# Performance work log

Measured on AMD Instinct MI355X. Metric: run time of the kernel, lower is better.

The kernel has to match this reference:

```python
import jax, jax.numpy as jnp
import numpy as np

N = 50000   # nodes
E = 800000  # edges (avg degree 16)
F = 64      # num_features (channels per irrep)
R = 8       # radial basis size
H = 64      # radial MLP hidden
S = 10      # num_species
NPATH = 5   # tensor-product paths: s*Y0->0, s*Y1->1, v*Y0->1, v.Y1->0, v x Y1->1
AVG_NEIGH = 16.0


def setup_inputs() -> dict:
    key = jax.random.key(0)
    ks = jax.random.split(key, 20)
    def w(k, shape, fan_in):
        return jax.random.normal(k, shape, dtype=jnp.float32) / np.sqrt(fan_in)
    return dict(
        vectors=jax.random.normal(ks[0], (E, 3), dtype=jnp.float32),
        node_feats_s=jax.random.normal(ks[1], (N, F), dtype=jnp.float32),
        node_feats_v=jax.random.normal(ks[2], (N, F, 3), dtype=jnp.float32),
        radial_embedding=jax.random.normal(ks[3], (E, R), dtype=jnp.float32),
        Wu_s=w(ks[7], (F, F), F), Wu_v=w(ks[8], (F, F), F),
        W_r1=w(ks[9], (R, H), R), W_r2=w(ks[10], (H, NPATH * F), H),
        Wd_s=w(ks[11], (F, F), F), Wd_v=w(ks[12], (F, F), F),
        w_sym_s=jax.random.normal(ks[13], (S, 3, F), dtype=jnp.float32),
        w_sym_v=jax.random.normal(ks[14], (S, 2, F), dtype=jnp.float32),
        WL_s=w(ks[15], (F, F), F), WL_v=w(ks[16], (F, F), F),
        W_skip_s=w(ks[17], (S, F, F), F), W_skip_v=w(ks[18], (S, F, F), F),
        W_out=w(ks[19], (F, 1), F),
        node_specie=jax.random.randint(ks[4], (N,), 0, S),
        senders=jax.random.randint(ks[5], (E,), 0, N),
        receivers=jax.random.randint(ks[6], (E,), 0, N),
    )


def reference(vectors, node_feats_s, node_feats_v, radial_embedding,
              Wu_s, Wu_v, W_r1, W_r2, Wd_s, Wd_v,
              w_sym_s, w_sym_v, WL_s, WL_v, W_skip_s, W_skip_v, W_out,
              node_specie, senders, receivers):
    n = node_feats_s.shape[0]
    # ---- self-connection: species-indexed linear (skip_tp), per-irrep channel mix
    sc_s = jnp.einsum('nf,nfg->ng', node_feats_s, W_skip_s[node_specie])
    sc_v = jnp.einsum('nfc,nfg->ngc', node_feats_v, W_skip_v[node_specie])
    # ---- InteractionBlock: linear up
    s = node_feats_s @ Wu_s                                  # [N,F]
    v = jnp.einsum('nfc,fg->ngc', node_feats_v, Wu_v)        # [N,F,3]
    # radial MLP -> per-edge, per-path, per-channel tensor-product weights
    h = jax.nn.silu(radial_embedding @ W_r1)
    w = (h @ W_r2).reshape(-1, NPATH, s.shape[1])            # [E,5,F]
    # spherical harmonics (l=1): unit edge vectors
    Y1 = vectors / (jnp.linalg.norm(vectors, axis=-1, keepdims=True) + 1e-9)  # [E,3]
    xs = s[senders]                                          # [E,F]
    xv = v[senders]                                          # [E,F,3]
    # CG tensor product paths (0e+1o) x (Y0+Y1) -> 0e + 1o
    m_s = w[:, 0] * xs + w[:, 3] * jnp.einsum('efc,ec->ef', xv, Y1)
    m_v = (w[:, 1, :, None] * xs[:, :, None] * Y1[:, None, :]
           + w[:, 2, :, None] * xv
           + w[:, 4, :, None] * jnp.cross(xv, Y1[:, None, :]))
    # scatter-sum aggregation over receivers
    agg_s = jax.ops.segment_sum(m_s, receivers, num_segments=n)
    agg_v = jax.ops.segment_sum(m_v, receivers, num_segments=n)
    # linear down to num_features * interaction_irreps
    s = agg_s @ Wd_s
    v = jnp.einsum('nfc,fg->ngc', agg_v, Wd_v)
    # epsilon is None -> divide by sqrt(avg_num_neighbors)
    inv = 1.0 / np.sqrt(AVG_NEIGH).astype(np.float32)
    s = s * inv
    v = v * inv
    # ---- EquivariantProductBasisBlock: symmetric contraction (correlation=2),
    # species-indexed per-channel weights over the symmetric CG basis
    ws = w_sym_s[node_specie]                                # [N,3,F]
    wv = w_sym_v[node_specie]                                # [N,2,F]
    ps = ws[:, 0] * s + ws[:, 1] * s * s + ws[:, 2] * jnp.sum(v * v, axis=-1)
    pv = wv[:, 0, :, None] * v + wv[:, 1, :, None] * (s[:, :, None] * v)
    # linear to num_features * hidden_irreps
    fs = ps @ WL_s
    fv = jnp.einsum('nfc,fg->ngc', pv, WL_v)
    # residual skip connection
    fs = fs + sc_s
    fv = fv + sc_v
    # ---- LinearReadoutBlock to output_irreps = '0e'
    node_outputs = fs @ W_out                                # [N,1]
    return node_outputs, fs, fv
```

## Files before the change

### kernel.cpp

```cpp
#include <hip/hip_runtime.h>
#include <stdint.h>

#define F 64
#define RDIM 8
#define HDIM 64
#define NPATH 5
#define EB 64
#define PADH 72
#define PADN 324
#define NSP 16
#define PB 72
#define NT 4

typedef _Float16 half8 __attribute__((ext_vector_type(8)));
typedef _Float16 half4 __attribute__((ext_vector_type(4)));
typedef float floatx4 __attribute__((ext_vector_type(4)));

#define ES_E(v)   ((int)((v) >> 32))
#define ES_R(v)   ((int)(((v) >> 16) & 0xFFFFu))
#define ES_S(v)   ((int)((v) & 0xFFFFu))

__device__ inline half8 h8_from_f32(const float* p) {
    float4 a = ((const float4*)p)[0];
    float4 b = ((const float4*)p)[1];
    half8 h;
    h[0] = (_Float16)a.x; h[1] = (_Float16)a.y; h[2] = (_Float16)a.z; h[3] = (_Float16)a.w;
    h[4] = (_Float16)b.x; h[5] = (_Float16)b.y; h[6] = (_Float16)b.z; h[7] = (_Float16)b.w;
    return h;
}

__device__ inline half8 h8_from_f32_stride3(const float* p) {
    half8 h;
#pragma unroll
    for (int j = 0; j < 8; ++j) h[j] = (_Float16)p[j * 3];
    return h;
}

__device__ inline half8 h8_zero() {
    half8 h;
#pragma unroll
    for (int j = 0; j < 8; ++j) h[j] = (_Float16)0.f;
    return h;
}

__global__ __launch_bounds__(256) void k_pre_mfma(
    const float* __restrict__ nfs, const float* __restrict__ nfv,
    const float* __restrict__ Wus, const float* __restrict__ Wuv,
    half4* __restrict__ comb, int N,
    const int* __restrict__ recv, int* __restrict__ cnt, int E,
    const int* __restrict__ specie, int* __restrict__ nbin)
{
    __shared__ _Float16 BT[2][64 * PB];
    __shared__ int lbin[NSP];
    const int tid = threadIdx.x;
    const int wave = tid >> 6, lane = tid & 63;
    const int l15 = lane & 15, lq = lane >> 4;
    const int tb0 = blockIdx.x * 64;

    if (tid < NSP) lbin[tid] = 0;
    {
        const float* srcs[2] = { Wus, Wuv };
#pragma unroll
        for (int m = 0; m < 2; ++m) {
            const float* W = srcs[m];
#pragma unroll
            for (int rep = 0; rep < 16; ++rep) {
                int id = rep * 256 + tid;
                int k = id >> 6, n = id & 63;
                BT[m][n * PB + k] = (_Float16)W[k * F + n];
            }
        }
    }
    __syncthreads();

    {
        const int i0 = blockIdx.x * 256 + tid;
        const int stride = gridDim.x * 256;
        for (int e = i0; e < E; e += stride) atomicAdd(&cnt[recv[e]], 1);
        for (int n = i0; n < N; n += stride) atomicAdd(&lbin[specie[n]], 1);
    }

    const int tb = tb0 + wave * 16;
    const int ndA = tb + l15;

#define BFRAG(m, nt, ks) (*(const half8*)&BT[m][((nt) * 16 + l15) * PB + (ks) * 32 + lq * 8])

    floatx4 c[4][NT];
#pragma unroll
    for (int q = 0; q < 4; ++q)
#pragma unroll
        for (int nt = 0; nt < NT; ++nt) c[q][nt] = (floatx4){0.f, 0.f, 0.f, 0.f};

#pragma unroll
    for (int ks = 0; ks < 2; ++ks) {
        half8 a_s, a_v0, a_v1, a_v2;
        if (ndA < N) {
            a_s  = h8_from_f32(nfs + (size_t)ndA * F + ks * 32 + lq * 8);
            const float* vb = nfv + ((size_t)ndA * F + ks * 32 + lq * 8) * 3;
            a_v0 = h8_from_f32_stride3(vb + 0);
            a_v1 = h8_from_f32_stride3(vb + 1);
            a_v2 = h8_from_f32_stride3(vb + 2);
        } else {
            a_s = a_v0 = a_v1 = a_v2 = h8_zero();
        }
#pragma unroll
        for (int nt = 0; nt < NT; ++nt) {
            half8 bs = BFRAG(0, nt, ks);
            half8 bv = BFRAG(1, nt, ks);
            c[0][nt] = __builtin_amdgcn_mfma_f32_16x16x32_f16(a_s,  bs, c[0][nt], 0, 0, 0);
            c[1][nt] = __builtin_amdgcn_mfma_f32_16x16x32_f16(a_v0, bv, c[1][nt], 0, 0, 0);
            c[2][nt] = __builtin_amdgcn_mfma_f32_16x16x32_f16(a_v1, bv, c[2][nt], 0, 0, 0);
            c[3][nt] = __builtin_amdgcn_mfma_f32_16x16x32_f16(a_v2, bv, c[3][nt], 0, 0, 0);
        }
    }
#undef BFRAG

#pragma unroll
    for (int r = 0; r < 4; ++r) {
        const int nd = tb + lq * 4 + r;
        if (nd < N) {
#pragma unroll
            for (int nt = 0; nt < NT; ++nt) {
                half4 o;
                o[0] = (_Float16)c[0][nt][r];
                o[1] = (_Float16)c[1][nt][r];
                o[2] = (_Float16)c[2][nt][r];
                o[3] = (_Float16)c[3][nt][r];
                comb[(size_t)nd * F + nt * 16 + l15] = o;
            }
        }
    }

    __syncthreads();
    if (tid < NSP && lbin[tid] > 0) atomicAdd(&nbin[tid], lbin[tid]);
}

__global__ __launch_bounds__(1024) void k_scanA(
    const int* __restrict__ cnt, int* __restrict__ bsum, int N)
{
    __shared__ int lsum[1024];
    const int tid = threadIdx.x;
    const int i = blockIdx.x * 1024 + tid;
    int x = (i < N) ? cnt[i] : 0;
    lsum[tid] = x;
    __syncthreads();
    for (int off = 512; off > 0; off >>= 1) {
        if (tid < off) lsum[tid] += lsum[tid + off];
        __syncthreads();
    }
    if (tid == 0) bsum[blockIdx.x] = lsum[0];
}

__global__ __launch_bounds__(64) void k_scanB(
    int* __restrict__ bsum, int nb,
    const int* __restrict__ nbin, int* __restrict__ ncur)
{
    const int lane = threadIdx.x;
    int carry = 0;
    for (int base = 0; base < nb; base += 64) {
        const int idx = base + lane;
        int v = (idx < nb) ? bsum[idx] : 0;
        int incl = v;
#pragma unroll
        for (int off = 1; off < 64; off <<= 1) {
            int u = __shfl_up(incl, off, 64);
            if (lane >= off) incl += u;
        }
        int tot = __shfl(incl, 63, 64);
        if (idx < nb) bsum[idx] = incl - v + carry;
        carry += tot;
    }
    if (lane == 0) {
        int run = 0;
        for (int s = 0; s < NSP; ++s) {
            ncur[s] = run;
            run += ((nbin[s] + 63) >> 6) << 6;
        }
    }
}

__global__ __launch_bounds__(1024) void k_scanC(
    const int* __restrict__ cnt, const int* __restrict__ bsum,
    int* __restrict__ cursor, int N)
{
    __shared__ int lsum[1024];
    const int tid = threadIdx.x;
    const int i = blockIdx.x * 1024 + tid;
    int x = (i < N) ? cnt[i] : 0;
    lsum[tid] = x;
    __syncthreads();
    int acc = x;
    for (int off = 1; off < 1024; off <<= 1) {
        int add = (tid >= off) ? lsum[tid - off] : 0;
        __syncthreads();
        acc += add;
        lsum[tid] = acc;
        __syncthreads();
    }
    if (i < N) cursor[i] = acc - x + bsum[blockIdx.x];
}

__global__ __launch_bounds__(256) void k_scatter(
    const int* __restrict__ recv, const int* __restrict__ send,
    int* __restrict__ cursor, unsigned long long* __restrict__ esort, int E,
    const int* __restrict__ specie, int* __restrict__ ncur,
    int* __restrict__ nperm, int N)
{
    __shared__ int lbin[NSP], lbase[NSP], lcur[NSP];
    const int tid = threadIdx.x;
    const int i0 = blockIdx.x * 256 + tid;
    const int stride = gridDim.x * 256;
    for (int e = i0; e < E; e += stride) {
        int r = recv[e];
        int p = atomicAdd(&cursor[r], 1);
        esort[p] = ((unsigned long long)(unsigned int)e << 32)
                 | ((unsigned long long)(unsigned int)r << 16)
                 | (unsigned long long)(unsigned int)send[e];
    }
    if (tid < NSP) { lbin[tid] = 0; lcur[tid] = 0; }
    __syncthreads();
    int sp = -1;
    if (i0 < N) { sp = specie[i0]; atomicAdd(&lbin[sp], 1); }
    __syncthreads();
    if (tid < NSP && lbin[tid] > 0) lbase[tid] = atomicAdd(&ncur[tid], lbin[tid]);
    __syncthreads();
    if (i0 < N) {
        int off = atomicAdd(&lcur[sp], 1);
        nperm[lbase[sp] + off] = i0;
    }
}

__global__ __launch_bounds__(256, 3) void k_edge(
    const float* __restrict__ vecs, const float* __restrict__ re,
    const float* __restrict__ Wr1, const float* __restrict__ Wr2,
    const unsigned long long* __restrict__ esort,
    const half4* __restrict__ comb,
    float* __restrict__ agg_s, float* __restrict__ agg_v, int E)
{
    __shared__ _Float16 h_lds[EB * PADH];
    __shared__ _Float16 w_lds[EB * PADN];
    const int tid = threadIdx.x;
    const int wave = tid >> 6, lane = tid & 63;
    const int l15 = lane & 15, lq = lane >> 4;

    half8 bfrag[5][2];
#pragma unroll
    for (int nt = 0; nt < 5; ++nt)
#pragma unroll
        for (int ks = 0; ks < 2; ++ks)
#pragma unroll
            for (int j = 0; j < 8; ++j) {
                int k = ks * 32 + lq * 8 + j;
                int n = wave * 80 + nt * 16 + l15;
                bfrag[nt][ks][j] = (_Float16)Wr2[k * (NPATH * F) + n];
            }

    float w1r[RDIM];
#pragma unroll
    for (int r = 0; r < RDIM; ++r) w1r[r] = Wr1[r * HDIM + lane];

    const int niter = (E + EB - 1) / EB;
    for (int it = blockIdx.x; it < niter; it += gridDim.x) {
        const int base = it * EB;
        const bool full = (base + EB <= E);

        if (full) {
            const int ew = base + wave * 16;
            unsigned long long es1[16];
#pragma unroll
            for (int j = 0; j < 8; ++j)
                ((int4*)es1)[j] = ((const int4*)(esort + ew))[j];
            float4 ra[4], rb[4];
#pragma unroll
            for (int j = 0; j < 4; ++j) {
                const float4* rp = (const float4*)(re + (size_t)ES_E(es1[j]) * RDIM);
                ra[j] = rp[0]; rb[j] = rp[1];
            }
#pragma unroll
            for (int t = 0; t < 16; ++t) {
                float4 A = ra[t & 3], B = rb[t & 3];
                if (t < 12) {
                    const float4* rp = (const float4*)(re + (size_t)ES_E(es1[t + 4]) * RDIM);
                    ra[t & 3] = rp[0]; rb[t & 3] = rp[1];
                }
                float h = A.x * w1r[0] + A.y * w1r[1] + A.z * w1r[2] + A.w * w1r[3]
                        + B.x * w1r[4] + B.y * w1r[5] + B.z * w1r[6] + B.w * w1r[7];
                h = h / (1.f + __expf(-h));
                h_lds[(wave * 16 + t) * PADH + lane] = (_Float16)h;
            }
        } else {
            for (int t = 0; t < 16; ++t) {
                const int eloc = wave * 16 + t;
                const int e = base + eloc;
                float h = 0.f;
                if (e < E) {
                    const int pe = ES_E(esort[e]);
                    const float4* rp = (const float4*)(re + (size_t)pe * RDIM);
                    float4 A = rp[0], B = rp[1];
                    h = A.x * w1r[0] + A.y * w1r[1] + A.z * w1r[2] + A.w * w1r[3]
                      + B.x * w1r[4] + B.y * w1r[5] + B.z * w1r[6] + B.w * w1r[7];
                    h = h / (1.f + __expf(-h));
                }
                h_lds[eloc * PADH + lane] = (_Float16)h;
            }
        }
        __syncthreads();

        floatx4 c[4][5];
#pragma unroll
        for (int mt = 0; mt < 4; ++mt)
#pragma unroll
            for (int nt = 0; nt < 5; ++nt)
                c[mt][nt] = (floatx4){0.f, 0.f, 0.f, 0.f};
#pragma unroll
        for (int ks = 0; ks < 2; ++ks) {
            half8 a[4];
#pragma unroll
            for (int mt = 0; mt < 4; ++mt)
                a[mt] = *(const half8*)&h_lds[(mt * 16 + l15) * PADH + ks * 32 + lq * 8];
#pragma unroll
            for (int mt = 0; mt < 4; ++mt)
#pragma unroll
                for (int nt = 0; nt < 5; ++nt)
                    c[mt][nt] = __builtin_amdgcn_mfma_f32_16x16x32_f16(
                        a[mt], bfrag[nt][ks], c[mt][nt], 0, 0, 0);
        }
#pragma unroll
        for (int mt = 0; mt < 4; ++mt)
#pragma unroll
            for (int nt = 0; nt < 5; ++nt)
#pragma unroll
                for (int r = 0; r < 4; ++r) {
                    int row = mt * 16 + lq * 4 + r;
                    int col = wave * 80 + nt * 16 + l15;
                    w_lds[row * PADN + col] = (_Float16)c[mt][nt][r];
                }
        __syncthreads();

        if (full) {
            const int ew = base + wave * 16;
            unsigned long long es[16];
#pragma unroll
            for (int j = 0; j < 8; ++j)
                ((int4*)es)[j] = ((const int4*)(esort + ew))[j];
            half4 gb[4];
            float vxr[4], vyr[4], vzr[4];
#pragma unroll
            for (int j = 0; j < 4; ++j) {
                gb[j] = comb[(size_t)ES_S(es[j]) * F + lane];
                const float* vp = vecs + (size_t)ES_E(es[j]) * 3;
                vxr[j] = vp[0]; vyr[j] = vp[1]; vzr[j] = vp[2];
            }
            float accs = 0.f, acc0 = 0.f, acc1 = 0.f, acc2 = 0.f;
            int cur = ES_R(es[0]);
#pragma unroll
            for (int t = 0; t < 16; ++t) {
                half4 g = gb[t & 3];
                float vx = vxr[t & 3], vy = vyr[t & 3], vz = vzr[t & 3];
                if (t < 12) {
                    gb[t & 3] = comb[(size_t)ES_S(es[t + 4]) * F + lane];
                    const float* vp = vecs + (size_t)ES_E(es[t + 4]) * 3;
                    vxr[t & 3] = vp[0]; vyr[t & 3] = vp[1]; vzr[t & 3] = vp[2];
                }
                const int eloc = wave * 16 + t;
                float nrm = sqrtf(vx * vx + vy * vy + vz * vz);
                float inv = 1.f / (nrm + 1e-9f);
                float Yx = vx * inv, Yy = vy * inv, Yz = vz * inv;
                float w0  = (float)w_lds[eloc * PADN + 0 * F + lane];
                float w1p = (float)w_lds[eloc * PADN + 1 * F + lane];
                float w2p = (float)w_lds[eloc * PADN + 2 * F + lane];
                float w3p = (float)w_lds[eloc * PADN + 3 * F + lane];
                float w4p = (float)w_lds[eloc * PADN + 4 * F + lane];
                float xs = (float)g[0], x0 = (float)g[1], x1 = (float)g[2], x2 = (float)g[3];
                float dvY = x0 * Yx + x1 * Yy + x2 * Yz;
                float ms = w0 * xs + w3p * dvY;
                float m0 = w1p * xs * Yx + w2p * x0 + w4p * (x1 * Yz - x2 * Yy);
                float m1 = w1p * xs * Yy + w2p * x1 + w4p * (x2 * Yx - x0 * Yz);
                float m2 = w1p * xs * Yz + w2p * x2 + w4p * (x0 * Yy - x1 * Yx);
                const int rt = ES_R(es[t]);
                if (rt != cur) {
                    float* asb = agg_s + (size_t)cur * F;
                    float* avb = agg_v + (size_t)cur * 3 * F;
                    unsafeAtomicAdd(&asb[lane], accs);
                    unsafeAtomicAdd(&avb[lane], acc0);
                    unsafeAtomicAdd(&avb[F + lane], acc1);
                    unsafeAtomicAdd(&avb[2 * F + lane], acc2);
                    accs = acc0 = acc1 = acc2 = 0.f;
                    cur = rt;
                }
                accs += ms; acc0 += m0; acc1 += m1; acc2 += m2;
            }
            {
                float* asb = agg_s + (size_t)cur * F;
                float* avb = agg_v + (size_t)cur * 3 * F;
                unsafeAtomicAdd(&asb[lane], accs);
                unsafeAtomicAdd(&avb[lane], acc0);
                unsafeAtomicAdd(&avb[F + lane], acc1);
                unsafeAtomicAdd(&avb[2 * F + lane], acc2);
            }
        } else {
            for (int t = 0; t < 16; ++t) {
                const int eloc = wave * 16 + t;
                const int e = base + eloc;
                if (e >= E) break;
                const unsigned long long ev = esort[e];
                const int pe = ES_E(ev), snd = ES_S(ev), rcv = ES_R(ev);
                const float* vp = vecs + (size_t)pe * 3;
                float vx = vp[0], vy = vp[1], vz = vp[2];
                float nrm = sqrtf(vx * vx + vy * vy + vz * vz);
                float inv = 1.f / (nrm + 1e-9f);
                float Yx = vx * inv, Yy = vy * inv, Yz = vz * inv;
                half4 g = comb[(size_t)snd * F + lane];
                float w0  = (float)w_lds[eloc * PADN + 0 * F + lane];
                float w1p = (float)w_lds[eloc * PADN + 1 * F + lane];
                float w2p = (float)w_lds[eloc * PADN + 2 * F + lane];
                float w3p = (float)w_lds[eloc * PADN + 3 * F + lane];
                float w4p = (float)w_lds[eloc * PADN + 4 * F + lane];
                float xs = (float)g[0], x0 = (float)g[1], x1 = (float)g[2], x2 = (float)g[3];
                float dvY = x0 * Yx + x1 * Yy + x2 * Yz;
                float ms = w0 * xs + w3p * dvY;
                float m0 = w1p * xs * Yx + w2p * x0 + w4p * (x1 * Yz - x2 * Yy);
                float m1 = w1p * xs * Yy + w2p * x1 + w4p * (x2 * Yx - x0 * Yz);
                float m2 = w1p * xs * Yz + w2p * x2 + w4p * (x0 * Yy - x1 * Yx);
                float* asb = agg_s + (size_t)rcv * F;
                float* avb = agg_v + (size_t)rcv * 3 * F;
                unsafeAtomicAdd(&asb[lane], ms);
                unsafeAtomicAdd(&avb[lane], m0);
                unsafeAtomicAdd(&avb[F + lane], m1);
                unsafeAtomicAdd(&avb[2 * F + lane], m2);
            }
        }
    }
}

__global__ __launch_bounds__(256) void k_post_mfma(
    const float* __restrict__ agg_s, const float* __restrict__ agg_v,
    const float* __restrict__ nfs, const float* __restrict__ nfv,
    const float* __restrict__ Wds, const float* __restrict__ Wdv,
    const float* __restrict__ wss, const float* __restrict__ wsv,
    const float* __restrict__ WLs, const float* __restrict__ WLv,
    const float* __restrict__ Wsks, const float* __restrict__ Wskv,
    const float* __restrict__ Wout, const int* __restrict__ specie,
    const int* __restrict__ nperm,
    float* __restrict__ out0, float* __restrict__ out_fs,
    float* __restrict__ out_fv, int N)
{
    __shared__ _Float16 BT[6][64 * PB];
    __shared__ _Float16 P_lds[4][16 * PB];
    const int tid = threadIdx.x;
    const int wave = tid >> 6, lane = tid & 63;
    const int l15 = lane & 15, lq = lane >> 4;
    const int tb0 = blockIdx.x * 64;

    const int nfirst = nperm[tb0];
    const int sp = (nfirst < 0) ? 0 : specie[nfirst];

    {
        const float* srcs[6] = { Wds, Wdv,
                                 Wsks + (size_t)sp * F * F, Wskv + (size_t)sp * F * F,
                                 WLs, WLv };
#pragma unroll
        for (int m = 0; m < 6; ++m) {
            const float* W = srcs[m];
#pragma unroll
            for (int rep = 0; rep < 16; ++rep) {
                int id = rep * 256 + tid;
                int k = id >> 6, n = id & 63;
                BT[m][n * PB + k] = (_Float16)W[k * F + n];
            }
        }
    }
    __syncthreads();

    const int tb = tb0 + wave * 16;
    const int ndA = nperm[tb + l15];
    int ndr[4];
#pragma unroll
    for (int r = 0; r < 4; ++r) ndr[r] = nperm[tb + lq * 4 + r];

#define BFRAG(m, nt, ks) (*(const half8*)&BT[m][((nt) * 16 + l15) * PB + (ks) * 32 + lq * 8])

    floatx4 csk[4][NT];
#pragma unroll
    for (int q = 0; q < 4; ++q)
#pragma unroll
        for (int nt = 0; nt < NT; ++nt) csk[q][nt] = (floatx4){0.f, 0.f, 0.f, 0.f};
#pragma unroll
    for (int ks = 0; ks < 2; ++ks) {
        half8 a_s, a_v0, a_v1, a_v2;
        if (ndA >= 0) {
            a_s  = h8_from_f32(nfs + (size_t)ndA * F + ks * 32 + lq * 8);
            const float* vb = nfv + ((size_t)ndA * F + ks * 32 + lq * 8) * 3;
            a_v0 = h8_from_f32_stride3(vb + 0);
            a_v1 = h8_from_f32_stride3(vb + 1);
            a_v2 = h8_from_f32_stride3(vb + 2);
        } else {
            a_s = a_v0 = a_v1 = a_v2 = h8_zero();
        }
#pragma unroll
        for (int nt = 0; nt < NT; ++nt) {
            half8 bs = BFRAG(2, nt, ks);
            half8 bv = BFRAG(3, nt, ks);
            csk[0][nt] = __builtin_amdgcn_mfma_f32_16x16x32_f16(a_s,  bs, csk[0][nt], 0, 0, 0);
            csk[1][nt] = __builtin_amdgcn_mfma_f32_16x16x32_f16(a_v0, bv, csk[1][nt], 0, 0, 0);
            csk[2][nt] = __builtin_amdgcn_mfma_f32_16x16x32_f16(a_v1, bv, csk[2][nt], 0, 0, 0);
            csk[3][nt] = __builtin_amdgcn_mfma_f32_16x16x32_f16(a_v2, bv, csk[3][nt], 0, 0, 0);
        }
    }

    floatx4 cdn[4][NT];
#pragma unroll
    for (int q = 0; q < 4; ++q)
#pragma unroll
        for (int nt = 0; nt < NT; ++nt) cdn[q][nt] = (floatx4){0.f, 0.f, 0.f, 0.f};
#pragma unroll
    for (int ks = 0; ks < 2; ++ks) {
        half8 a_s, a_v0, a_v1, a_v2;
        if (ndA >= 0) {
            a_s  = h8_from_f32(agg_s + (size_t)ndA * F + ks * 32 + lq * 8);
            const float* vb = agg_v + (size_t)ndA * 3 * F + ks * 32 + lq * 8;
            a_v0 = h8_from_f32(vb);
            a_v1 = h8_from_f32(vb + F);
            a_v2 = h8_from_f32(vb + 2 * F);
        } else {
            a_s = a_v0 = a_v1 = a_v2 = h8_zero();
        }
#pragma unroll
        for (int nt = 0; nt < NT; ++nt) {
            half8 bs = BFRAG(0, nt, ks);
            half8 bv = BFRAG(1, nt, ks);
            cdn[0][nt] = __builtin_amdgcn_mfma_f32_16x16x32_f16(a_s,  bs, cdn[0][nt], 0, 0, 0);
            cdn[1][nt] = __builtin_amdgcn_mfma_f32_16x16x32_f16(a_v0, bv, cdn[1][nt], 0, 0, 0);
            cdn[2][nt] = __builtin_amdgcn_mfma_f32_16x16x32_f16(a_v1, bv, cdn[2][nt], 0, 0, 0);
            cdn[3][nt] = __builtin_amdgcn_mfma_f32_16x16x32_f16(a_v2, bv, cdn[3][nt], 0, 0, 0);
        }
    }

#pragma unroll
    for (int nt = 0; nt < NT; ++nt) {
        const int g = nt * 16 + l15;
        float a0 = wss[(sp * 3 + 0) * F + g];
        float a1 = wss[(sp * 3 + 1) * F + g];
        float a2 = wss[(sp * 3 + 2) * F + g];
        float b0 = wsv[(sp * 2 + 0) * F + g];
        float b1 = wsv[(sp * 2 + 1) * F + g];
#pragma unroll
        for (int r = 0; r < 4; ++r) {
            const float inv = 0.25f;
            float s2  = cdn[0][nt][r] * inv;
            float v20 = cdn[1][nt][r] * inv;
            float v21 = cdn[2][nt][r] * inv;
            float v22 = cdn[3][nt][r] * inv;
            cdn[0][nt][r] = a0 * s2 + a1 * s2 * s2
                          + a2 * (v20 * v20 + v21 * v21 + v22 * v22);
            cdn[1][nt][r] = b0 * v20 + b1 * s2 * v20;
            cdn[2][nt][r] = b0 * v21 + b1 * s2 * v21;
            cdn[3][nt][r] = b0 * v22 + b1 * s2 * v22;
        }
    }

#pragma unroll
    for (int q = 0; q < 4; ++q) {
#pragma unroll
        for (int nt = 0; nt < NT; ++nt)
#pragma unroll
            for (int r = 0; r < 4; ++r)
                P_lds[wave][(lq * 4 + r) * PB + nt * 16 + l15] = (_Float16)cdn[q][nt][r];
        __syncthreads();
        half8 ap0 = *(const half8*)&P_lds[wave][l15 * PB + 0 * 32 + lq * 8];
        half8 ap1 = *(const half8*)&P_lds[wave][l15 * PB + 1 * 32 + lq * 8];
        const int bm = (q == 0) ? 4 : 5;
#pragma unroll
        for (int nt = 0; nt < NT; ++nt) {
            csk[q][nt] = __builtin_amdgcn_mfma_f32_16x16x32_f16(ap0, BFRAG(bm, nt, 0), csk[q][nt], 0, 0, 0);
            csk[q][nt] = __builtin_amdgcn_mfma_f32_16x16x32_f16(ap1, BFRAG(bm, nt, 1), csk[q][nt], 0, 0, 0);
        }
        __syncthreads();
    }
#undef BFRAG

    float wo[NT];
#pragma unroll
    for (int nt = 0; nt < NT; ++nt) wo[nt] = Wout[nt * 16 + l15];
#pragma unroll
    for (int r = 0; r < 4; ++r) {
        const int nd = ndr[r];
        float po = 0.f;
        if (nd >= 0) {
#pragma unroll
            for (int nt = 0; nt < NT; ++nt) {
                const int g = nt * 16 + l15;
                float fs = csk[0][nt][r];
                out_fs[(size_t)nd * F + g] = fs;
                po += fs * wo[nt];
                float* fvp = out_fv + ((size_t)nd * F + g) * 3;
                fvp[0] = csk[1][nt][r];
                fvp[1] = csk[2][nt][r];
                fvp[2] = csk[3][nt][r];
            }
            po += __shfl_xor(po, 1, 64);
            po += __shfl_xor(po, 2, 64);
            po += __shfl_xor(po, 4, 64);
            po += __shfl_xor(po, 8, 64);
            if (l15 == 0) out0[nd] = po;
        }
    }
}

extern "C" void kernel_launch(void* const* d_in, const int* in_sizes, int n_in,
                              void* d_out, int out_size, void* d_ws, size_t ws_size,
                              hipStream_t stream)
{
    const float* vectors = (const float*)d_in[0];
    const float* nfs  = (const float*)d_in[1];
    const float* nfv  = (const float*)d_in[2];
    const float* re   = (const float*)d_in[3];
    const float* Wus  = (const float*)d_in[4];
    const float* Wuv  = (const float*)d_in[5];
    const float* Wr1  = (const float*)d_in[6];
    const float* Wr2  = (const float*)d_in[7];
    const float* Wds  = (const float*)d_in[8];
    const float* Wdv  = (const float*)d_in[9];
    const float* wss  = (const float*)d_in[10];
    const float* wsv  = (const float*)d_in[11];
    const float* WLs  = (const float*)d_in[12];
    const float* WLv  = (const float*)d_in[13];
    const float* Wsks = (const float*)d_in[14];
    const float* Wskv = (const float*)d_in[15];
    const float* Wout = (const float*)d_in[16];
    const int* specie    = (const int*)d_in[17];
    const int* senders   = (const int*)d_in[18];
    const int* receivers = (const int*)d_in[19];

    const int N = in_sizes[1] / F;
    const int E = in_sizes[18];

    const size_t NF = (size_t)N * F;
    const int NPAD_MAX = N + NSP * 64 + 64;
    half4* comb  = (half4*)d_ws;
    float* agg_s = (float*)((char*)d_ws + NF * sizeof(half4));
    float* agg_v = agg_s + NF;
    unsigned long long* esort = (unsigned long long*)(agg_v + 3 * NF);
    int*   cnt    = (int*)(esort + E);
    int*   nbin   = cnt + N;
    int*   ncur   = nbin + NSP;
    int*   cursor = ncur + NSP;
    int*   bsum   = cursor + N;
    int*   nperm  = bsum + 64;

    hipMemsetAsync(agg_s, 0, (size_t)4 * NF * sizeof(float), stream);
    hipMemsetAsync(cnt, 0, (size_t)(N + NSP) * sizeof(int), stream);
    hipMemsetAsync(nperm, 0xFF, (size_t)NPAD_MAX * sizeof(int), stream);

    const int nb64 = (N + 63) / 64;
    const int nbs = (N + 1023) / 1024;
    const int nbp = (N + NSP * 64 + 63) / 64;

    k_pre_mfma<<<nb64, 256, 0, stream>>>(nfs, nfv, Wus, Wuv, comb, N,
                                         receivers, cnt, E, specie, nbin);
    k_scanA<<<nbs, 1024, 0, stream>>>(cnt, bsum, N);
    k_scanB<<<1, 64, 0, stream>>>(bsum, nbs, nbin, ncur);
    k_scanC<<<nbs, 1024, 0, stream>>>(cnt, bsum, cursor, N);
    k_scatter<<<1024, 256, 0, stream>>>(receivers, senders, cursor, esort, E,
                                        specie, ncur, nperm, N);
    k_edge<<<2048, 256, 0, stream>>>(vectors, re, Wr1, Wr2, esort,
                                     comb, agg_s, agg_v, E);
    float* out0   = (float*)d_out;
    float* out_fs = out0 + N;
    float* out_fv = out_fs + (size_t)N * F;
    k_post_mfma<<<nbp, 256, 0, stream>>>(agg_s, agg_v, nfs, nfv, Wds, Wdv,
                                         wss, wsv, WLs, WLv, Wsks, Wskv,
                                         Wout, specie, nperm,
                                         out0, out_fs, out_fv, N);
}
```

Measured before the change: 542.1 us.

## Fuse scan and scatter kernels into one cooperative kernel with grid syncs

Merges the three-stage prefix scan (block sums, carry scan, per-block scan) and the edge/node scatter into a single cooperative kernel. Grid-wide syncs replace the kernel boundaries, and the scan chunk size drops from 1024 to 256. The goal is to remove three kernel launches and their gaps in a small, launch-bound preprocessing phase. The cost is a cooperative launch, grid.sync overhead, and the requirement that all 1024 blocks be co-resident, plus a larger bsum region.

```diff
diff --git a/kernel.cpp b/kernel.cpp
--- a/kernel.cpp
+++ b/kernel.cpp
@@ -1,5 +1,8 @@
 #include <hip/hip_runtime.h>
+#include <hip/hip_cooperative_groups.h>
 #include <stdint.h>
+
+namespace cg = cooperative_groups;
 
 #define F 64
 #define RDIM 8
@@ -11,6 +14,7 @@
 #define NSP 16
 #define PB 72
 #define NT 4
+#define SORT_BLOCKS 1024
 
 typedef _Float16 half8 __attribute__((ext_vector_type(8)));
 typedef _Float16 half4 __attribute__((ext_vector_type(4)));
@@ -135,79 +139,78 @@
     if (tid < NSP && lbin[tid] > 0) atomicAdd(&nbin[tid], lbin[tid]);
 }
 
-__global__ __launch_bounds__(1024) void k_scanA(
-    const int* __restrict__ cnt, int* __restrict__ bsum, int N)
+__global__ __launch_bounds__(256) void k_sort(
+    const int* __restrict__ cnt, int* __restrict__ bsum,
+    int* __restrict__ cursor,
+    const int* __restrict__ recv, const int* __restrict__ send,
+    unsigned long long* __restrict__ esort,
+    const int* __restrict__ specie, const int* __restrict__ nbin,
+    int* __restrict__ ncur, int* __restrict__ nperm, int N, int E)
 {
-    __shared__ int lsum[1024];
-    const int tid = threadIdx.x;
-    const int i = blockIdx.x * 1024 + tid;
-    int x = (i < N) ? cnt[i] : 0;
-    lsum[tid] = x;
-    __syncthreads();
-    for (int off = 512; off > 0; off >>= 1) {
-        if (tid < off) lsum[tid] += lsum[tid + off];
-        __syncthreads();
-    }
-    if (tid == 0) bsum[blockIdx.x] = lsum[0];
-}
-
-__global__ __launch_bounds__(64) void k_scanB(
-    int* __restrict__ bsum, int nb,
-    const int* __restrict__ nbin, int* __restrict__ ncur)
-{
-    const int lane = threadIdx.x;
-    int carry = 0;
-    for (int base = 0; base < nb; base += 64) {
-        const int idx = base + lane;
-        int v = (idx < nb) ? bsum[idx] : 0;
-        int incl = v;
-#pragma unroll
-        for (int off = 1; off < 64; off <<= 1) {
-            int u = __shfl_up(incl, off, 64);
-            if (lane >= off) incl += u;
-        }
-        int tot = __shfl(incl, 63, 64);
-        if (idx < nb) bsum[idx] = incl - v + carry;
-        carry += tot;
-    }
-    if (lane == 0) {
-        int run = 0;
-        for (int s = 0; s < NSP; ++s) {
-            ncur[s] = run;
-            run += ((nbin[s] + 63) >> 6) << 6;
-        }
-    }
-}
-
-__global__ __launch_bounds__(1024) void k_scanC(
-    const int* __restrict__ cnt, const int* __restrict__ bsum,
-    int* __restrict__ cursor, int N)
-{
-    __shared__ int lsum[1024];
-    const int tid = threadIdx.x;
-    const int i = blockIdx.x * 1024 + tid;
-    int x = (i < N) ? cnt[i] : 0;
-    lsum[tid] = x;
-    __syncthreads();
-    int acc = x;
-    for (int off = 1; off < 1024; off <<= 1) {
-        int add = (tid >= off) ? lsum[tid - off] : 0;
-        __syncthreads();
-        acc += add;
-        lsum[tid] = acc;
-        __syncthreads();
-    }
-    if (i < N) cursor[i] = acc - x + bsum[blockIdx.x];
-}
-
-__global__ __launch_bounds__(256) void k_scatter(
-    const int* __restrict__ recv, const int* __restrict__ send,
-    int* __restrict__ cursor, unsigned long long* __restrict__ esort, int E,
-    const int* __restrict__ specie, int* __restrict__ ncur,
-    int* __restrict__ nperm, int N)
-{
+    cg::grid_group grid = cg::this_grid();
+    __shared__ int lsum[256];
     __shared__ int lbin[NSP], lbase[NSP], lcur[NSP];
     const int tid = threadIdx.x;
+    const int nch = (N + 255) >> 8;
+
+    for (int ch = blockIdx.x; ch < nch; ch += gridDim.x) {
+        const int i = ch * 256 + tid;
+        int x = (i < N) ? cnt[i] : 0;
+        lsum[tid] = x;
+        __syncthreads();
+        for (int off = 128; off > 0; off >>= 1) {
+            if (tid < off) lsum[tid] += lsum[tid + off];
+            __syncthreads();
+        }
+        if (tid == 0) bsum[ch] = lsum[0];
+        __syncthreads();
+    }
+    grid.sync();
+
+    if (blockIdx.x == 0 && tid < 64) {
+        const int lane = tid;
+        int carry = 0;
+        for (int base = 0; base < nch; base += 64) {
+            const int idx = base + lane;
+            int v = (idx < nch) ? bsum[idx] : 0;
+            int incl = v;
+#pragma unroll
+            for (int off = 1; off < 64; off <<= 1) {
+                int u = __shfl_up(incl, off, 64);
+                if (lane >= off) incl += u;
+            }
+            int tot = __shfl(incl, 63, 64);
+            if (idx < nch) bsum[idx] = incl - v + carry;
+            carry += tot;
+        }
+        if (lane == 0) {
+            int run = 0;
+            for (int s = 0; s < NSP; ++s) {
+                ncur[s] = run;
+                run += ((nbin[s] + 63) >> 6) << 6;
+            }
+        }
+    }
+    grid.sync();
+
+    for (int ch = blockIdx.x; ch < nch; ch += gridDim.x) {
+        const int i = ch * 256 + tid;
+        int x = (i < N) ? cnt[i] : 0;
+        lsum[tid] = x;
+        __syncthreads();
+        int acc = x;
+        for (int off = 1; off < 256; off <<= 1) {
+            int add = (tid >= off) ? lsum[tid - off] : 0;
+            __syncthreads();
+            acc += add;
+            lsum[tid] = acc;
+            __syncthreads();
+        }
+        if (i < N) cursor[i] = acc - x + bsum[ch];
+        __syncthreads();
+    }
+    grid.sync();
+
     const int i0 = blockIdx.x * 256 + tid;
     const int stride = gridDim.x * 256;
     for (int e = i0; e < E; e += stride) {
@@ -632,8 +635,8 @@
     const int* senders   = (const int*)d_in[18];
     const int* receivers = (const int*)d_in[19];
 
-    const int N = in_sizes[1] / F;
-    const int E = in_sizes[18];
+    int N = in_sizes[1] / F;
+    int E = in_sizes[18];
 
     const size_t NF = (size_t)N * F;
     const int NPAD_MAX = N + NSP * 64 + 64;
@@ -646,23 +649,27 @@
     int*   ncur   = nbin + NSP;
     int*   cursor = ncur + NSP;
     int*   bsum   = cursor + N;
-    int*   nperm  = bsum + 64;
+    int*   nperm  = bsum + 256;
 
     hipMemsetAsync(agg_s, 0, (size_t)4 * NF * sizeof(float), stream);
     hipMemsetAsync(cnt, 0, (size_t)(N + NSP) * sizeof(int), stream);
     hipMemsetAsync(nperm, 0xFF, (size_t)NPAD_MAX * sizeof(int), stream);
 
     const int nb64 = (N + 63) / 64;
-    const int nbs = (N + 1023) / 1024;
     const int nbp = (N + NSP * 64 + 63) / 64;
 
     k_pre_mfma<<<nb64, 256, 0, stream>>>(nfs, nfv, Wus, Wuv, comb, N,
                                          receivers, cnt, E, specie, nbin);
-    k_scanA<<<nbs, 1024, 0, stream>>>(cnt, bsum, N);
-    k_scanB<<<1, 64, 0, stream>>>(bsum, nbs, nbin, ncur);
-    k_scanC<<<nbs, 1024, 0, stream>>>(cnt, bsum, cursor, N);
-    k_scatter<<<1024, 256, 0, stream>>>(receivers, senders, cursor, esort, E,
-                                        specie, ncur, nperm, N);
+
+    {
+        void* sargs[] = { (void*)&cnt, (void*)&bsum, (void*)&cursor,
+                          (void*)&receivers, (void*)&senders, (void*)&esort,
+                          (void*)&specie, (void*)&nbin, (void*)&ncur,
+                          (void*)&nperm, (void*)&N, (void*)&E };
+        hipLaunchCooperativeKernel((void*)k_sort, dim3(SORT_BLOCKS), dim3(256),
+                                   sargs, 0, stream);
+    }
+
     k_edge<<<2048, 256, 0, stream>>>(vectors, re, Wr1, Wr2, esort,
                                      comb, agg_s, agg_v, E);
     float* out0   = (float*)d_out;
```

After: 824.9 us. 1.52x slower.
